# Kernel tuning notes

Measured on AMD Instinct MI355X. Metric: run time of the kernel, lower is better.

The kernel has to match this reference:

```python
import jax, jax.numpy as jnp
import numpy as np

N_NODES = 100000
N_EDGES = 1600000
D_IN = 128
D_OUT = 128


def setup_inputs() -> dict:
    key = jax.random.key(0)
    k1, k2, k3, k4 = jax.random.split(key, 4)
    x = jax.random.normal(k1, (N_NODES, D_IN), dtype=jnp.float32)
    edge_index = jax.random.randint(k2, (2, N_EDGES), 0, N_NODES, dtype=jnp.int64)
    # Xavier-uniform init as in the torch module
    limit = float(np.sqrt(6.0 / (D_IN + D_OUT)))
    self_weight = jax.random.uniform(k3, (D_IN, D_OUT), dtype=jnp.float32, minval=-limit, maxval=limit)
    neighbor_weight = jax.random.uniform(k4, (D_IN, D_OUT), dtype=jnp.float32, minval=-limit, maxval=limit)
    bias = jnp.zeros((D_OUT,), dtype=jnp.float32)
    return {"x": x, "edge_index": edge_index, "self_weight": self_weight,
            "neighbor_weight": neighbor_weight, "bias": bias}


def reference(x, edge_index, self_weight, neighbor_weight, bias):
    row, col = edge_index[0], edge_index[1]
    num_nodes = x.shape[0]
    # symmetric normalization: deg^-1/2 over rows, gathered per edge
    deg = jax.ops.segment_sum(jnp.ones_like(row, dtype=x.dtype), row,
                              num_segments=num_nodes)
    deg_inv_sqrt = deg ** -0.5
    norm = deg_inv_sqrt[row] * deg_inv_sqrt[col]  # [E]
    # dense transforms
    self_support = x @ self_weight                 # [N, D_OUT]
    h = x @ neighbor_weight                        # [N, D_OUT]
    # spmm: out[r] += norm_e * h[c] for each edge (r, c)
    msg = norm[:, None] * h[col]                   # [E, D_OUT]
    neighbor_support = jax.ops.segment_sum(msg, row, num_segments=num_nodes)
    return self_support + neighbor_support + bias
```

## Files before the change

### kernel.cpp

```cpp
#include <hip/hip_runtime.h>

#define N_NODES 100000
#define N_EDGES 1600000
#define D_FEAT 128
#define BUCKETS 1024
#define RPB 98
#define BKCAP 2048
#define BIN_CHUNK 4096
#define BIN_WGS ((N_EDGES + BIN_CHUNK - 1) / BIN_CHUNK)

#define CONV_ELEMS (N_NODES * D_FEAT / 4)
#define CONV_WGS 2048

#define WPREP_WGS 16
#define KBIN_WGS (WPREP_WGS + BIN_WGS)

typedef unsigned int u32;
typedef unsigned short u16;
typedef __attribute__((ext_vector_type(8))) short bf16x8;
typedef __attribute__((ext_vector_type(4))) float f32x4;

__device__ inline float bfbits2f(u32 hi) { union { u32 u; float f; } v; v.u = hi; return v.f; }
__device__ inline float bflo(u32 pair) { return bfbits2f(pair << 16); }
__device__ inline float bfhi(u32 pair) { return bfbits2f(pair & 0xFFFF0000u); }
__device__ inline u16 f2bf(float f) {
  union { float f; u32 u; } v; v.f = f;
  u32 r = v.u + 0x7FFFu + ((v.u >> 16) & 1u);
  return (u16)(r >> 16);
}
__device__ inline int clampN(int v) { return ((unsigned)v < N_NODES) ? v : 0; }

__global__ __launch_bounds__(256) void k_conv(const float4* __restrict__ x4,
                                              uint2* __restrict__ xb2,
                                              int* __restrict__ gcur) {
  if (blockIdx.x == 0) {
#pragma unroll
    for (int k = 0; k < BUCKETS / 256; k++) gcur[k * 256 + threadIdx.x] = 0;
  }
  for (int i = blockIdx.x * 256 + threadIdx.x; i < CONV_ELEMS; i += CONV_WGS * 256) {
    float4 v = x4[i];
    uint2 o;
    o.x = (u32)f2bf(v.x) | ((u32)f2bf(v.y) << 16);
    o.y = (u32)f2bf(v.z) | ((u32)f2bf(v.w) << 16);
    xb2[i] = o;
  }
}

__global__ __launch_bounds__(256) void k_bin(const float* __restrict__ Wself,
                                             const float* __restrict__ Wnb,
                                             u16* __restrict__ Wbf,
                                             const int* __restrict__ ei,
                                             int* __restrict__ gcur,
                                             u32* __restrict__ binrec) {
  __shared__ int hist[BUCKETS], pref[BUCKETS], lcur[BUCKETS], ps[256];
  __shared__ u32 stag[BIN_CHUNK];
  __shared__ u16 sbkt[BIN_CHUNK];
  int b = blockIdx.x;
  int tid = threadIdx.x;
  if (b < WPREP_WGS) {
    int f = b * 256 + tid;
    int lane = f & 63, nt = (f >> 6) & 7, kk = (f >> 9) & 3, t = f >> 11;
    int q = lane >> 4, l16 = lane & 15;
    const float* W = t ? Wnb : Wself;
    int n = nt * 16 + l16;
    int k0 = (kk * 4 + q) * 8;
    u16 tmp[8];
#pragma unroll
    for (int j = 0; j < 8; j++) tmp[j] = f2bf(W[(k0 + j) * 128 + n]);
    uint4 o;
    o.x = (u32)tmp[0] | ((u32)tmp[1] << 16);
    o.y = (u32)tmp[2] | ((u32)tmp[3] << 16);
    o.z = (u32)tmp[4] | ((u32)tmp[5] << 16);
    o.w = (u32)tmp[6] | ((u32)tmp[7] << 16);
    *(uint4*)(Wbf + (long)f * 8) = o;
  } else {
    int wb = b - WPREP_WGS;
    long e0 = (long)wb * BIN_CHUNK;
    for (int k = tid; k < BUCKETS; k += 256) { hist[k] = 0; lcur[k] = 0; }
    __syncthreads();
    int rows[BIN_CHUNK / 256];
#pragma unroll
    for (int j = 0; j < BIN_CHUNK / 256; j++) {
      long e = e0 + j * 256 + tid;
      int r = (e < N_EDGES) ? clampN(ei[e]) : -1;
      rows[j] = r;
      if (r >= 0) atomicAdd(&hist[r / RPB], 1);
    }
    __syncthreads();
    int v0 = hist[4 * tid + 0], v1 = hist[4 * tid + 1];
    int v2 = hist[4 * tid + 2], v3 = hist[4 * tid + 3];
    int s = v0 + v1 + v2 + v3;
    ps[tid] = s;
    __syncthreads();
    for (int off = 1; off < 256; off <<= 1) {
      int t = (tid >= off) ? ps[tid - off] : 0;
      __syncthreads();
      ps[tid] += t;
      __syncthreads();
    }
    int excl = ps[tid] - s;
    pref[4 * tid + 0] = excl;
    pref[4 * tid + 1] = excl + v0;
    pref[4 * tid + 2] = excl + v0 + v1;
    pref[4 * tid + 3] = excl + v0 + v1 + v2;
    hist[4 * tid + 0] = (4 * tid + 0) * BKCAP + (v0 ? atomicAdd(&gcur[4 * tid + 0], v0) : 0);
    hist[4 * tid + 1] = (4 * tid + 1) * BKCAP + (v1 ? atomicAdd(&gcur[4 * tid + 1], v1) : 0);
    hist[4 * tid + 2] = (4 * tid + 2) * BKCAP + (v2 ? atomicAdd(&gcur[4 * tid + 2], v2) : 0);
    hist[4 * tid + 3] = (4 * tid + 3) * BKCAP + (v3 ? atomicAdd(&gcur[4 * tid + 3], v3) : 0);
    int total = ps[255];
    __syncthreads();
#pragma unroll
    for (int j = 0; j < BIN_CHUNK / 256; j++) {
      int r = rows[j];
      if (r < 0) continue;
      long e = e0 + j * 256 + tid;
      int c = clampN(ei[N_EDGES + e]);
      int bk = r / RPB;
      int rl = r - bk * RPB;
      int pos = pref[bk] + atomicAdd(&lcur[bk], 1);
      stag[pos] = ((u32)rl << 17) | (u32)c;
      sbkt[pos] = (u16)bk;
    }
    __syncthreads();
    for (int i = tid; i < total; i += 256) {
      int bk = sbkt[i];
      int idx = hist[bk] + (i - pref[bk]);
      if (idx < (bk + 1) * BKCAP) binrec[idx] = stag[i];
    }
  }
}

__global__ __launch_bounds__(256) void k_csr(const int* __restrict__ gcur,
                                             const u32* __restrict__ binrec,
                                             int* __restrict__ deg,
                                             int* __restrict__ row_start,
                                             float* __restrict__ dis,
                                             int* __restrict__ cn) {
  __shared__ int h[128];
  __shared__ int cur[128];
  __shared__ int win[BKCAP];
  int tid = threadIdx.x;
  int b = blockIdx.x;
  int r0 = b * RPB;
  int nrows = N_NODES - r0; if (nrows > RPB) nrows = RPB;
  int base = b * BKCAP;
  int cnt = gcur[b]; if (cnt > BKCAP) cnt = BKCAP;
  if (tid < 128) h[tid] = 0;
  __syncthreads();
  for (int i = tid; i < cnt; i += 256) {
    u32 rec = binrec[base + i];
    atomicAdd(&h[rec >> 17], 1);
  }
  __syncthreads();
  int v = (tid < 128) ? h[tid] : 0;
  __syncthreads();
  for (int off = 1; off < 128; off <<= 1) {
    int t = (tid >= off && tid < 128) ? h[tid - off] : 0;
    __syncthreads();
    if (tid < 128) h[tid] += t;
    __syncthreads();
  }
  int excl = (tid < 128) ? (h[tid] - v) : 0;
  if (tid < 128) cur[tid] = excl;
  if (tid < nrows) {
    int r = r0 + tid;
    deg[r] = v;
    row_start[r] = base + excl;
    dis[r] = v ? rsqrtf((float)v) : 0.0f;
  }
  __syncthreads();
  for (int i = tid; i < cnt; i += 256) {
    u32 rec = binrec[base + i];
    int rl = rec >> 17;
    int p = atomicAdd(&cur[rl], 1);
    win[p] = (int)(rec & 0x1FFFF);
  }
  __syncthreads();
  for (int i = tid; i < cnt; i += 256) cn[base + i] = win[i];
}

__global__ __launch_bounds__(256) void k_agg(const int* __restrict__ row_start,
                                             const int* __restrict__ deg,
                                             const float* __restrict__ dis,
                                             const int* __restrict__ cn,
                                             const u32* __restrict__ xb ,
                                             u32* __restrict__ aggb) {
  int wave = threadIdx.x >> 6, lane = threadIdx.x & 63;
  int r = blockIdx.x * 4 + wave;
  if (r >= N_NODES) return;
  int start = row_start[r];
  int cnt = deg[r];
  float dr = dis[r];
  float a0 = 0.f, a1 = 0.f, b0 = 0.f, b1 = 0.f;
  int i = 0;
  for (; i + 8 <= cnt; i += 8) {
    int c[8];
    u32 g[8];
    float nc[8];
#pragma unroll
    for (int j = 0; j < 8; j++) c[j] = cn[start + i + j];
#pragma unroll
    for (int j = 0; j < 8; j++) g[j] = xb[(long)c[j] * 64 + lane];
#pragma unroll
    for (int j = 0; j < 8; j++) nc[j] = dis[c[j]];
#pragma unroll
    for (int j = 0; j < 8; j++) {
      float n = dr * nc[j];
      if (j & 1) { b0 += n * bflo(g[j]); b1 += n * bfhi(g[j]); }
      else       { a0 += n * bflo(g[j]); a1 += n * bfhi(g[j]); }
    }
  }
  for (; i + 2 <= cnt; i += 2) {
    int c0 = cn[start + i], c1 = cn[start + i + 1];
    u32 g0 = xb[(long)c0 * 64 + lane];
    u32 g1 = xb[(long)c1 * 64 + lane];
    float n0 = dr * dis[c0], n1 = dr * dis[c1];
    a0 += n0 * bflo(g0); a1 += n0 * bfhi(g0);
    b0 += n1 * bflo(g1); b1 += n1 * bfhi(g1);
  }
  if (i < cnt) {
    int c0 = cn[start + i];
    u32 g0 = xb[(long)c0 * 64 + lane];
    float n0 = dr * dis[c0];
    a0 += n0 * bflo(g0); a1 += n0 * bfhi(g0);
  }
  a0 += b0; a1 += b1;
  aggb[(long)r * 64 + lane] = (u32)f2bf(a0) | ((u32)f2bf(a1) << 16);
}

__global__ __launch_bounds__(256) void k_gemm(const u16* __restrict__ xb,
                                              const u16* __restrict__ aggb,
                                              const u16* __restrict__ Wbf,
                                              const float* __restrict__ bias,
                                              float* __restrict__ out) {
  int tid = threadIdx.x;
  int wave = tid >> 6, lane = tid & 63;
  int q = lane >> 4, l16 = lane & 15;
  int w0 = blockIdx.x * 128 + wave * 32;

  bf16x8 ax[2][4], ag[2][4];
#pragma unroll
  for (int mt = 0; mt < 2; mt++) {
    int node = w0 + mt * 16 + l16;
    long aoff = (long)clampN(node) * D_FEAT + q * 8;
#pragma unroll
    for (int kk = 0; kk < 4; kk++) {
      ax[mt][kk] = *(const bf16x8*)(xb + aoff + kk * 32);
      ag[mt][kk] = *(const bf16x8*)(aggb + aoff + kk * 32);
    }
  }

#pragma unroll
  for (int nt = 0; nt < 8; nt++) {
    bf16x8 bs[4], bn[4];
#pragma unroll
    for (int kk = 0; kk < 4; kk++) {
      bs[kk] = *(const bf16x8*)(Wbf + (long)(((0 * 4 + kk) * 8 + nt) * 64 + lane) * 8);
      bn[kk] = *(const bf16x8*)(Wbf + (long)(((1 * 4 + kk) * 8 + nt) * 64 + lane) * 8);
    }
    int ncol = nt * 16 + l16;
    float bv = bias[ncol];
#pragma unroll
    for (int mt = 0; mt < 2; mt++) {
      f32x4 acc = {0.f, 0.f, 0.f, 0.f};
#pragma unroll
      for (int kk = 0; kk < 4; kk++)
        acc = __builtin_amdgcn_mfma_f32_16x16x32_bf16(ax[mt][kk], bs[kk], acc, 0, 0, 0);
#pragma unroll
      for (int kk = 0; kk < 4; kk++)
        acc = __builtin_amdgcn_mfma_f32_16x16x32_bf16(ag[mt][kk], bn[kk], acc, 0, 0, 0);
#pragma unroll
      for (int reg = 0; reg < 4; reg++) {
        int node = w0 + mt * 16 + q * 4 + reg;
        if (node < N_NODES) out[(long)node * D_FEAT + ncol] = acc[reg] + bv;
      }
    }
  }
}

extern "C" void kernel_launch(void* const* d_in, const int* in_sizes, int n_in,
                              void* d_out, int out_size, void* d_ws, size_t ws_size,
                              hipStream_t stream) {
  const float* x = (const float*)d_in[0];
  const int* ei = (const int*)d_in[1];
  const float* Wself = (const float*)d_in[2];
  const float* Wnb = (const float*)d_in[3];
  const float* bias = (const float*)d_in[4];
  float* out = (float*)d_out;

  auto alignup = [](size_t v) { return (v + 511) & ~(size_t)511; };
  char* p = (char*)d_ws;
  int* deg = (int*)p;            p += alignup((size_t)N_NODES * 4);
  int* row_start = (int*)p;      p += alignup((size_t)N_NODES * 4);
  float* dis = (float*)p;        p += alignup((size_t)N_NODES * 4);
  int* gcur = (int*)p;           p += alignup((size_t)BUCKETS * 4);
  u16* Wbf = (u16*)p;            p += alignup((size_t)4096 * 8 * 2);
  int* cn = (int*)p;             p += alignup((size_t)BUCKETS * BKCAP * 4);
  u16* xb = (u16*)p;             p += alignup((size_t)N_NODES * D_FEAT * 2);
  u16* aggb = (u16*)p;           p += alignup((size_t)N_NODES * D_FEAT * 2);
  u32* binrec = (u32*)d_out;

  k_conv<<<CONV_WGS, 256, 0, stream>>>((const float4*)x, (uint2*)xb, gcur);
  k_bin<<<KBIN_WGS, 256, 0, stream>>>(Wself, Wnb, Wbf, ei, gcur, binrec);
  k_csr<<<BUCKETS, 256, 0, stream>>>(gcur, binrec, deg, row_start, dis, cn);
  k_agg<<<(N_NODES + 3) / 4, 256, 0, stream>>>(row_start, deg, dis, cn, (const u32*)xb, (u32*)aggb);
  k_gemm<<<(N_NODES + 127) / 128, 256, 0, stream>>>(xb, aggb, Wbf, bias, out);
}
```

Baseline: 254.9 us.

## Fuse neighbor aggregation and dual GEMM into one kernel via LDS

Merges the sparse aggregation and the MFMA GEMM into a single kernel. Each 512-thread workgroup aggregates 16 rows (two per wave) into padded shared memory, then each wave computes one 16-column tile of the output. This removes the aggb round-trip through global memory and one kernel launch. In exchange, weights are reloaded per 16-row block instead of being amortized over 128 rows, and each wave now aggregates two rows serially, which can raise per-block latency.

```diff
diff --git a/kernel.cpp b/kernel.cpp
--- a/kernel.cpp
+++ b/kernel.cpp
@@ -14,6 +14,9 @@
 
 #define WPREP_WGS 16
 #define KBIN_WGS (WPREP_WGS + BIN_WGS)
+
+#define AGG_STRIDE 68
+#define AGEMM_WGS (N_NODES / 16)
 
 typedef unsigned int u32;
 typedef unsigned short u16;
@@ -179,102 +182,86 @@
   for (int i = tid; i < cnt; i += 256) cn[base + i] = win[i];
 }
 
-__global__ __launch_bounds__(256) void k_agg(const int* __restrict__ row_start,
-                                             const int* __restrict__ deg,
-                                             const float* __restrict__ dis,
-                                             const int* __restrict__ cn,
-                                             const u32* __restrict__ xb ,
-                                             u32* __restrict__ aggb) {
+__global__ __launch_bounds__(512) void k_aggemm(const int* __restrict__ row_start,
+                                                const int* __restrict__ deg,
+                                                const float* __restrict__ dis,
+                                                const int* __restrict__ cn,
+                                                const u32* __restrict__ xb ,
+                                                const u16* __restrict__ Wbf,
+                                                const float* __restrict__ bias,
+                                                float* __restrict__ out) {
+  __shared__ u32 agg[16 * AGG_STRIDE];
   int wave = threadIdx.x >> 6, lane = threadIdx.x & 63;
-  int r = blockIdx.x * 4 + wave;
-  if (r >= N_NODES) return;
-  int start = row_start[r];
-  int cnt = deg[r];
-  float dr = dis[r];
-  float a0 = 0.f, a1 = 0.f, b0 = 0.f, b1 = 0.f;
-  int i = 0;
-  for (; i + 8 <= cnt; i += 8) {
-    int c[8];
-    u32 g[8];
-    float nc[8];
-#pragma unroll
-    for (int j = 0; j < 8; j++) c[j] = cn[start + i + j];
-#pragma unroll
-    for (int j = 0; j < 8; j++) g[j] = xb[(long)c[j] * 64 + lane];
-#pragma unroll
-    for (int j = 0; j < 8; j++) nc[j] = dis[c[j]];
-#pragma unroll
-    for (int j = 0; j < 8; j++) {
-      float n = dr * nc[j];
-      if (j & 1) { b0 += n * bflo(g[j]); b1 += n * bfhi(g[j]); }
-      else       { a0 += n * bflo(g[j]); a1 += n * bfhi(g[j]); }
-    }
-  }
-  for (; i + 2 <= cnt; i += 2) {
-    int c0 = cn[start + i], c1 = cn[start + i + 1];
-    u32 g0 = xb[(long)c0 * 64 + lane];
-    u32 g1 = xb[(long)c1 * 64 + lane];
-    float n0 = dr * dis[c0], n1 = dr * dis[c1];
-    a0 += n0 * bflo(g0); a1 += n0 * bfhi(g0);
-    b0 += n1 * bflo(g1); b1 += n1 * bfhi(g1);
-  }
-  if (i < cnt) {
-    int c0 = cn[start + i];
-    u32 g0 = xb[(long)c0 * 64 + lane];
-    float n0 = dr * dis[c0];
-    a0 += n0 * bflo(g0); a1 += n0 * bfhi(g0);
-  }
-  a0 += b0; a1 += b1;
-  aggb[(long)r * 64 + lane] = (u32)f2bf(a0) | ((u32)f2bf(a1) << 16);
-}
-
-__global__ __launch_bounds__(256) void k_gemm(const u16* __restrict__ xb,
-                                              const u16* __restrict__ aggb,
-                                              const u16* __restrict__ Wbf,
-                                              const float* __restrict__ bias,
-                                              float* __restrict__ out) {
-  int tid = threadIdx.x;
-  int wave = tid >> 6, lane = tid & 63;
+  int nb0 = blockIdx.x * 16;
+
+#pragma unroll 1
+  for (int t = 0; t < 2; t++) {
+    int rl = wave * 2 + t;
+    int r = nb0 + rl;
+    int start = row_start[r];
+    int cnt = deg[r];
+    float dr = dis[r];
+    float a0 = 0.f, a1 = 0.f, b0 = 0.f, b1 = 0.f;
+    int i = 0;
+    for (; i + 8 <= cnt; i += 8) {
+      int c[8];
+      u32 g[8];
+      float nc[8];
+#pragma unroll
+      for (int j = 0; j < 8; j++) c[j] = cn[start + i + j];
+#pragma unroll
+      for (int j = 0; j < 8; j++) g[j] = xb[(long)c[j] * 64 + lane];
+#pragma unroll
+      for (int j = 0; j < 8; j++) nc[j] = dis[c[j]];
+#pragma unroll
+      for (int j = 0; j < 8; j++) {
+        float n = dr * nc[j];
+        if (j & 1) { b0 += n * bflo(g[j]); b1 += n * bfhi(g[j]); }
+        else       { a0 += n * bflo(g[j]); a1 += n * bfhi(g[j]); }
+      }
+    }
+    for (; i + 2 <= cnt; i += 2) {
+      int c0 = cn[start + i], c1 = cn[start + i + 1];
+      u32 g0 = xb[(long)c0 * 64 + lane];
+      u32 g1 = xb[(long)c1 * 64 + lane];
+      float n0 = dr * dis[c0], n1 = dr * dis[c1];
+      a0 += n0 * bflo(g0); a1 += n0 * bfhi(g0);
+      b0 += n1 * bflo(g1); b1 += n1 * bfhi(g1);
+    }
+    if (i < cnt) {
+      int c0 = cn[start + i];
+      u32 g0 = xb[(long)c0 * 64 + lane];
+      float n0 = dr * dis[c0];
+      a0 += n0 * bflo(g0); a1 += n0 * bfhi(g0);
+    }
+    a0 += b0; a1 += b1;
+    agg[rl * AGG_STRIDE + lane] = (u32)f2bf(a0) | ((u32)f2bf(a1) << 16);
+  }
+  __syncthreads();
+
   int q = lane >> 4, l16 = lane & 15;
-  int w0 = blockIdx.x * 128 + wave * 32;
-
-  bf16x8 ax[2][4], ag[2][4];
-#pragma unroll
-  for (int mt = 0; mt < 2; mt++) {
-    int node = w0 + mt * 16 + l16;
-    long aoff = (long)clampN(node) * D_FEAT + q * 8;
-#pragma unroll
-    for (int kk = 0; kk < 4; kk++) {
-      ax[mt][kk] = *(const bf16x8*)(xb + aoff + kk * 32);
-      ag[mt][kk] = *(const bf16x8*)(aggb + aoff + kk * 32);
-    }
-  }
-
-#pragma unroll
-  for (int nt = 0; nt < 8; nt++) {
-    bf16x8 bs[4], bn[4];
-#pragma unroll
-    for (int kk = 0; kk < 4; kk++) {
-      bs[kk] = *(const bf16x8*)(Wbf + (long)(((0 * 4 + kk) * 8 + nt) * 64 + lane) * 8);
-      bn[kk] = *(const bf16x8*)(Wbf + (long)(((1 * 4 + kk) * 8 + nt) * 64 + lane) * 8);
-    }
-    int ncol = nt * 16 + l16;
-    float bv = bias[ncol];
-#pragma unroll
-    for (int mt = 0; mt < 2; mt++) {
-      f32x4 acc = {0.f, 0.f, 0.f, 0.f};
-#pragma unroll
-      for (int kk = 0; kk < 4; kk++)
-        acc = __builtin_amdgcn_mfma_f32_16x16x32_bf16(ax[mt][kk], bs[kk], acc, 0, 0, 0);
-#pragma unroll
-      for (int kk = 0; kk < 4; kk++)
-        acc = __builtin_amdgcn_mfma_f32_16x16x32_bf16(ag[mt][kk], bn[kk], acc, 0, 0, 0);
-#pragma unroll
-      for (int reg = 0; reg < 4; reg++) {
-        int node = w0 + mt * 16 + q * 4 + reg;
-        if (node < N_NODES) out[(long)node * D_FEAT + ncol] = acc[reg] + bv;
-      }
-    }
+  int nt = wave;
+  int ncol = nt * 16 + l16;
+  float bv = bias[ncol];
+  const u16* xb16 = (const u16*)xb;
+
+  f32x4 acc = {0.f, 0.f, 0.f, 0.f};
+#pragma unroll
+  for (int kk = 0; kk < 4; kk++) {
+    bf16x8 ax = *(const bf16x8*)(xb16 + (long)(nb0 + l16) * D_FEAT + q * 8 + kk * 32);
+    bf16x8 bs = *(const bf16x8*)(Wbf + (long)((kk * 8 + nt) * 64 + lane) * 8);
+    acc = __builtin_amdgcn_mfma_f32_16x16x32_bf16(ax, bs, acc, 0, 0, 0);
+  }
+#pragma unroll
+  for (int kk = 0; kk < 4; kk++) {
+    bf16x8 av = *(const bf16x8*)((const u16*)&agg[l16 * AGG_STRIDE + q * 4 + kk * 16]);
+    bf16x8 bn = *(const bf16x8*)(Wbf + (long)(((4 + kk) * 8 + nt) * 64 + lane) * 8);
+    acc = __builtin_amdgcn_mfma_f32_16x16x32_bf16(av, bn, acc, 0, 0, 0);
+  }
+#pragma unroll
+  for (int reg = 0; reg < 4; reg++) {
+    int nd = nb0 + q * 4 + reg;
+    out[(long)nd * D_FEAT + ncol] = acc[reg] + bv;
   }
 }
 
@@ -297,12 +284,10 @@
   u16* Wbf = (u16*)p;            p += alignup((size_t)4096 * 8 * 2);
   int* cn = (int*)p;             p += alignup((size_t)BUCKETS * BKCAP * 4);
   u16* xb = (u16*)p;             p += alignup((size_t)N_NODES * D_FEAT * 2);
-  u16* aggb = (u16*)p;           p += alignup((size_t)N_NODES * D_FEAT * 2);
   u32* binrec = (u32*)d_out;
 
   k_conv<<<CONV_WGS, 256, 0, stream>>>((const float4*)x, (uint2*)xb, gcur);
   k_bin<<<KBIN_WGS, 256, 0, stream>>>(Wself, Wnb, Wbf, ei, gcur, binrec);
   k_csr<<<BUCKETS, 256, 0, stream>>>(gcur, binrec, deg, row_start, dis, cn);
-  k_agg<<<(N_NODES + 3) / 4, 256, 0, stream>>>(row_start, deg, dis, cn, (const u32*)xb, (u32*)aggb);
-  k_gemm<<<(N_NODES + 127) / 128, 256, 0, stream>>>(xb, aggb, Wbf, bias, out);
-}
+  k_aggemm<<<AGEMM_WGS, 512, 0, stream>>>(row_start, deg, dis, cn, (const u32*)xb, Wbf, bias, out);
+}
```

New measurement: 268.5 us. +5.4%, slower.
